# Performance work log

Measured on AMD Instinct MI355X. Metric: run time of the kernel, lower is better.

Reference implementation:

```python
import jax, jax.numpy as jnp
import numpy as np

N_NODES = 100000
N_EDGES = 1600000
IN_FEATS, H_FEATS, NUM_CLASSES = 128, 64, 16


def setup_inputs() -> dict:
    key = jax.random.key(0)
    k1, k2, k3, k4, k5, k6, k7 = jax.random.split(key, 7)
    in_feat = jax.random.normal(k1, (N_NODES, IN_FEATS), dtype=jnp.float32)
    src = jax.random.randint(k2, (N_EDGES,), 0, N_NODES)
    dst = jax.random.randint(k3, (N_EDGES,), 0, N_NODES)
    # GraphConv parameters (glorot-ish scale)
    W1 = jax.random.normal(k4, (IN_FEATS, H_FEATS), dtype=jnp.float32) * (1.0 / np.sqrt(IN_FEATS))
    b1 = jnp.zeros((H_FEATS,), dtype=jnp.float32)
    W2 = jax.random.normal(k5, (H_FEATS, NUM_CLASSES), dtype=jnp.float32) * (1.0 / np.sqrt(H_FEATS))
    b2 = jnp.zeros((NUM_CLASSES,), dtype=jnp.float32)
    return {"in_feat": in_feat, "src": src, "dst": dst, "W1": W1, "b1": b1, "W2": W2, "b2": b2}


def reference(in_feat, src, dst, W1, b1, W2, b2):
    N = in_feat.shape[0]
    ones = jnp.ones(src.shape[0], dtype=in_feat.dtype)
    deg_out = jax.ops.segment_sum(ones, src, num_segments=N)
    deg_in = jax.ops.segment_sum(ones, dst, num_segments=N)
    # norm='both': deg^{-1/2}, degree clamped to >= 1 (allow_zero_in_degree)
    norm_out = jnp.maximum(deg_out, 1.0) ** -0.5  # [N]
    norm_in = jnp.maximum(deg_in, 1.0) ** -0.5    # [N]

    def gconv(x, W, b):
        x = x * norm_out[:, None]          # pre-normalize by src degree
        x = x @ W                          # project first (in_feats >= out_feats)
        msg = x[src]                       # gather [E, d_out]
        agg = jax.ops.segment_sum(msg, dst, num_segments=N)  # scatter-add [N, d_out]
        return agg * norm_in[:, None] + b  # post-normalize + bias

    h = jax.nn.relu(gconv(in_feat, W1, b1))
    h = gconv(h, W2, b2)
    return jnp.mean(h, axis=0)  # dgl.mean_nodes over single graph -> [num_classes]
```

## Files before the change

kernel.cpp:

```cpp
#include <hip/hip_runtime.h>
#include <hip/hip_fp16.h>

#define IN_F 128
#define H_F 64
#define C_F 16
#define BUCKET 256
#define BSH 8
#define MAXB 512
#define EPB 8192
#define AGG_W 64
#define CAP 2048
#define NRED 64
#define AK 136

typedef __attribute__((ext_vector_type(8))) short short8v;
typedef __attribute__((ext_vector_type(4))) float f32x4;

static __device__ inline short f2bf(float f) {
    unsigned u = __float_as_uint(f);
    unsigned r = (u + 0x7FFFu + ((u >> 16) & 1u)) >> 16;
    return (short)r;
}

__global__ __launch_bounds__(256) void k_bhist(const int* __restrict__ src,
                                               const int* __restrict__ dst,
                                               int* __restrict__ cntS,
                                               int* __restrict__ cntD, int E, int nb) {
    __shared__ int hs[MAXB];
    __shared__ int hd[MAXB];
    const int tid = threadIdx.x;
    for (int i = tid; i < MAXB; i += 256) { hs[i] = 0; hd[i] = 0; }
    __syncthreads();
    const int start = blockIdx.x * EPB;
    for (int k = 0; k < EPB / 256; ++k) {
        int e = start + (k << 8) + tid;
        if (e < E) {
            atomicAdd(&hs[src[e] >> BSH], 1);
            atomicAdd(&hd[dst[e] >> BSH], 1);
        }
    }
    __syncthreads();
    for (int b = tid; b < nb; b += 256) {
        int s = hs[b], d = hd[b];
        if (s) atomicAdd(&cntS[b], s);
        if (d) atomicAdd(&cntD[b], d);
    }
}

__global__ __launch_bounds__(1024) void k_bucketscan2(const int* __restrict__ cntD,
                                                      const int* __restrict__ cntS,
                                                      int* __restrict__ baseD,
                                                      int* __restrict__ curD,
                                                      int* __restrict__ baseS,
                                                      int* __restrict__ curS,
                                                      int nb, int E) {
    __shared__ int s[1024];
    const int t = threadIdx.x;
    for (int pass = 0; pass < 2; ++pass) {
        const int* cnt = pass ? cntS : cntD;
        int* base = pass ? baseS : baseD;
        int* cur  = pass ? curS  : curD;
        int i0 = 2 * t, i1 = 2 * t + 1;
        int v0 = (i0 < nb) ? cnt[i0] : 0;
        int v1 = (i1 < nb) ? cnt[i1] : 0;
        int pair = v0 + v1;
        s[t] = pair;
        __syncthreads();
        for (int off = 1; off < 1024; off <<= 1) {
            int x = (t >= off) ? s[t - off] : 0;
            __syncthreads();
            s[t] += x;
            __syncthreads();
        }
        int excl = s[t] - pair;
        if (i0 < nb) { base[i0] = excl;      cur[i0] = excl; }
        if (i1 < nb) { base[i1] = excl + v0; cur[i1] = excl + v0; }
        if (t == 0) base[nb] = E;
        __syncthreads();
    }
}

__global__ __launch_bounds__(256) void k_bin2(const int* __restrict__ src,
                                              const int* __restrict__ dst,
                                              int* __restrict__ gCurD,
                                              int* __restrict__ gCurS,
                                              unsigned int* __restrict__ binnedD,
                                              unsigned int* __restrict__ binnedS,
                                              int E, int nb) {
    __shared__ int hd[MAXB], hs[MAXB];
    __shared__ int bd[MAXB], bs[MAXB];
    __shared__ int cd[MAXB], cs[MAXB];
    const int tid = threadIdx.x;
    const int start = blockIdx.x * EPB;
    for (int i = tid; i < MAXB; i += 256) { hd[i] = 0; hs[i] = 0; cd[i] = 0; cs[i] = 0; }
    __syncthreads();
    for (int k = 0; k < EPB / 256; ++k) {
        int e = start + (k << 8) + tid;
        if (e < E) {
            atomicAdd(&hd[dst[e] >> BSH], 1);
            atomicAdd(&hs[src[e] >> BSH], 1);
        }
    }
    __syncthreads();
    for (int b = tid; b < nb; b += 256) {
        if (hd[b]) bd[b] = atomicAdd(&gCurD[b], hd[b]);
        if (hs[b]) bs[b] = atomicAdd(&gCurS[b], hs[b]);
    }
    __syncthreads();
    for (int k = 0; k < EPB / 256; ++k) {
        int e = start + (k << 8) + tid;
        if (e < E) {
            int sv = src[e], dv = dst[e];
            int b1 = dv >> BSH;
            int p1 = bd[b1] + atomicAdd(&cd[b1], 1);
            binnedD[p1] = ((unsigned)(dv & (BUCKET - 1)) << 17) | (unsigned)sv;
            int b2 = sv >> BSH;
            int p2 = bs[b2] + atomicAdd(&cs[b2], 1);
            binnedS[p2] = ((unsigned)(sv & (BUCKET - 1)) << 17) | (unsigned)dv;
        }
    }
}

__global__ __launch_bounds__(256) void k_sortD(const unsigned int* __restrict__ binnedD,
                                               const int* __restrict__ baseD,
                                               int* __restrict__ sortedSrc,
                                               int* __restrict__ nodeOff,
                                               float* __restrict__ norm_in,
                                               int N, int E) {
    __shared__ int hist[BUCKET];
    __shared__ int cur[BUCKET];
    __shared__ int wtot[4];
    const int tid = threadIdx.x, lane = tid & 63, wave = tid >> 6;
    const int b = blockIdx.x;
    const int s0 = baseD[b], s1 = baseD[b + 1];

    hist[tid] = 0;
    __syncthreads();
    for (int i = s0 + tid; i < s1; i += 256)
        atomicAdd(&hist[binnedD[i] >> 17], 1);
    __syncthreads();

    int v = hist[tid];
    int inc = v;
#pragma unroll
    for (int off = 1; off < 64; off <<= 1) {
        int t2 = __shfl_up(inc, off);
        if (lane >= off) inc += t2;
    }
    if (lane == 63) wtot[wave] = inc;
    __syncthreads();
    int add = 0;
#pragma unroll
    for (int w2 = 0; w2 < 4; ++w2)
        if (w2 < wave) add += wtot[w2];
    int excl = add + inc - v;
    cur[tid] = s0 + excl;
    int gn = b * BUCKET + tid;
    if (gn < N) {
        nodeOff[gn] = s0 + excl;
        norm_in[gn] = 1.0f / sqrtf((float)max(v, 1));
        if (gn == N - 1) nodeOff[N] = E;
    }
    __syncthreads();

    for (int i = s0 + tid; i < s1; i += 256) {
        unsigned c = binnedD[i];
        int p = atomicAdd(&cur[c >> 17], 1);
        sortedSrc[p] = (int)(c & 0x1FFFFu);
    }
}

__global__ __launch_bounds__(256) void k_wsum(const unsigned int* __restrict__ binnedS,
                                              const int* __restrict__ baseS,
                                              const float* __restrict__ norm_in,
                                              float* __restrict__ wsum,
                                              float* __restrict__ norm_out, int N) {
    __shared__ float wloc[BUCKET];
    __shared__ int hist[BUCKET];
    const int tid = threadIdx.x;
    wloc[tid] = 0.0f;
    hist[tid] = 0;
    __syncthreads();
    const int b = blockIdx.x;
    const int s0 = baseS[b], s1 = baseS[b + 1];
    for (int i = s0 + tid; i < s1; i += 256) {
        unsigned c = binnedS[i];
        int sl = (int)(c >> 17);
        float ni = norm_in[c & 0x1FFFFu];
        atomicAdd(&hist[sl], 1);
        atomicAdd(&wloc[sl], ni);
    }
    __syncthreads();
    int gn = b * BUCKET + tid;
    if (gn < N) {
        norm_out[gn] = 1.0f / sqrtf((float)max(hist[tid], 1));
        wsum[gn] = wloc[tid];
    }
}

__global__ __launch_bounds__(256) void k_gemm1(const float* __restrict__ in_feat,
                                               const float* __restrict__ W1,
                                               const float* __restrict__ norm_out,
                                               unsigned char* __restrict__ X1q, int N) {
    __shared__ union {
        short a[64][AK];
        float c[64][68];
    } u;
    __shared__ short wt[64][AK];
    const int t = threadIdx.x;
    const int lane = t & 63, wave = t >> 6;
    const int base = blockIdx.x * 64;

    for (int i = t; i < IN_F * H_F; i += 256) {
        int k = i >> 6, n = i & 63;
        wt[n][k] = f2bf(W1[i]);
    }
    for (int i = t; i < 64 * IN_F / 4; i += 256) {
        int n = i >> 5, k4 = (i & 31) * 4;
        int gn = base + n;
        float4 v = make_float4(0.f, 0.f, 0.f, 0.f);
        if (gn < N) v = *(const float4*)(in_feat + (size_t)gn * IN_F + k4);
        short4 s4 = make_short4(f2bf(v.x), f2bf(v.y), f2bf(v.z), f2bf(v.w));
        *(short4*)&u.a[n][k4] = s4;
    }
    __syncthreads();

    f32x4 acc0 = {}, acc1 = {}, acc2 = {}, acc3 = {};
    const int rowb = wave * 16 + (lane & 15);
    const int ko = (lane >> 4) * 8;
#pragma unroll
    for (int kk = 0; kk < 4; ++kk) {
        short8v af = *(const short8v*)&u.a[rowb][kk * 32 + ko];
        short8v b0 = *(const short8v*)&wt[0 + (lane & 15)][kk * 32 + ko];
        short8v b1f = *(const short8v*)&wt[16 + (lane & 15)][kk * 32 + ko];
        short8v b2 = *(const short8v*)&wt[32 + (lane & 15)][kk * 32 + ko];
        short8v b3 = *(const short8v*)&wt[48 + (lane & 15)][kk * 32 + ko];
        acc0 = __builtin_amdgcn_mfma_f32_16x16x32_bf16(af, b0, acc0, 0, 0, 0);
        acc1 = __builtin_amdgcn_mfma_f32_16x16x32_bf16(af, b1f, acc1, 0, 0, 0);
        acc2 = __builtin_amdgcn_mfma_f32_16x16x32_bf16(af, b2, acc2, 0, 0, 0);
        acc3 = __builtin_amdgcn_mfma_f32_16x16x32_bf16(af, b3, acc3, 0, 0, 0);
    }
    __syncthreads();

    {
        const int col = lane & 15;
        const int row0 = wave * 16 + (lane >> 4) * 4;
#pragma unroll
        for (int r = 0; r < 4; ++r) {
            u.c[row0 + r][col +  0] = acc0[r];
            u.c[row0 + r][col + 16] = acc1[r];
            u.c[row0 + r][col + 32] = acc2[r];
            u.c[row0 + r][col + 48] = acc3[r];
        }
    }
    __syncthreads();

    {
        int n = t >> 2, fq = (t & 3) * 16;
        int gn = base + n;
        if (gn < N) {
            float no = norm_out[gn];
            unsigned pk[4];
#pragma unroll
            for (int q = 0; q < 4; ++q) {
                int f = fq + q * 4;
                int w0 = 0;
                w0 = __builtin_amdgcn_cvt_pk_fp8_f32(u.c[n][f + 0] * no, u.c[n][f + 1] * no, w0, false);
                w0 = __builtin_amdgcn_cvt_pk_fp8_f32(u.c[n][f + 2] * no, u.c[n][f + 3] * no, w0, true);
                pk[q] = (unsigned)w0;
            }
            *(uint4*)&X1q[(size_t)gn * 64 + fq] = make_uint4(pk[0], pk[1], pk[2], pk[3]);
        }
    }
}

__global__ __launch_bounds__(256) void k_agg(const unsigned char* __restrict__ X1q,
                                             const int* __restrict__ sortedSrc,
                                             const int* __restrict__ nodeOff,
                                             const float* __restrict__ norm_in,
                                             const float* __restrict__ norm_out,
                                             const float* __restrict__ wsum,
                                             const float* __restrict__ b1,
                                             float* __restrict__ partials, int N) {
    __shared__ int ids[CAP];
    __shared__ int noff[AGG_W + 1];
    __shared__ float hl[4][64];
    const int tid = threadIdx.x, lane = tid & 63, wave = tid >> 6;
    const int fq = (lane & 15) * 4;
    const int eo = lane >> 4;
    const int gbase = blockIdx.x * AGG_W;
    const int nend = (gbase + AGG_W < N) ? gbase + AGG_W : N;
    const int nloc = nend - gbase;

    if (tid <= nloc) noff[tid] = nodeOff[gbase + tid];
    __syncthreads();
    const int s0 = noff[0];
    const int cnt = noff[nloc] - s0;
    const bool fast = (cnt <= CAP);
    if (fast) {
        for (int i = tid; i < cnt; i += 256) ids[i] = sortedSrc[s0 + i];
    }
    __syncthreads();

    const float bj0 = b1[fq + 0], bj1 = b1[fq + 1];
    const float bj2 = b1[fq + 2], bj3 = b1[fq + 3];
    float h0 = 0.f, h1 = 0.f, h2 = 0.f, h3 = 0.f;

    for (int k = 0; k < 16; ++k) {
        int nl = wave * 16 + k;
        if (nl >= nloc) break;
        int gn = gbase + nl;
        int e0 = noff[nl] - s0, e1 = noff[nl + 1] - s0;
        float a0 = 0.f, a1 = 0.f, a2 = 0.f, a3 = 0.f;
        for (int e = e0; e < e1; e += 16) {
            int sv[4];
            unsigned qv[4];
#pragma unroll
            for (int u = 0; u < 4; ++u) {
                int ee = e + 4 * u + eo;
                sv[u] = (ee < e1) ? (fast ? ids[ee] : sortedSrc[s0 + ee]) : -1;
            }
#pragma unroll
            for (int u = 0; u < 4; ++u)
                qv[u] = (sv[u] >= 0) ? *(const unsigned*)&X1q[(size_t)sv[u] * 64 + fq] : 0u;
#pragma unroll
            for (int u = 0; u < 4; ++u) {
                a0 += __builtin_amdgcn_cvt_f32_fp8(qv[u], 0);
                a1 += __builtin_amdgcn_cvt_f32_fp8(qv[u], 1);
                a2 += __builtin_amdgcn_cvt_f32_fp8(qv[u], 2);
                a3 += __builtin_amdgcn_cvt_f32_fp8(qv[u], 3);
            }
        }
        a0 += __shfl_xor(a0, 16); a0 += __shfl_xor(a0, 32);
        a1 += __shfl_xor(a1, 16); a1 += __shfl_xor(a1, 32);
        a2 += __shfl_xor(a2, 16); a2 += __shfl_xor(a2, 32);
        a3 += __shfl_xor(a3, 16); a3 += __shfl_xor(a3, 32);
        float ni = norm_in[gn];
        float w  = norm_out[gn] * wsum[gn];
        float v0 = a0 * ni + bj0, v1 = a1 * ni + bj1;
        float v2 = a2 * ni + bj2, v3 = a3 * ni + bj3;
        h0 = fmaf(v0 > 0.f ? v0 : 0.f, w, h0);
        h1 = fmaf(v1 > 0.f ? v1 : 0.f, w, h1);
        h2 = fmaf(v2 > 0.f ? v2 : 0.f, w, h2);
        h3 = fmaf(v3 > 0.f ? v3 : 0.f, w, h3);
    }
    if (lane < 16) {
        hl[wave][fq + 0] = h0; hl[wave][fq + 1] = h1;
        hl[wave][fq + 2] = h2; hl[wave][fq + 3] = h3;
    }
    __syncthreads();
    if (wave == 0)
        partials[(size_t)blockIdx.x * 64 + lane] =
            (hl[0][lane] + hl[1][lane]) + (hl[2][lane] + hl[3][lane]);
}

__global__ __launch_bounds__(256) void k_red(const float* __restrict__ partials,
                                             double* __restrict__ red, int nbp) {
    const int lane = threadIdx.x & 63, wave = threadIdx.x >> 6;
    const int rpb = (nbp + NRED - 1) / NRED;
    const int r0 = blockIdx.x * rpb;
    int r1 = r0 + rpb; if (r1 > nbp) r1 = nbp;
    double s = 0.0;
    for (int r = r0 + wave; r < r1; r += 4)
        s += (double)partials[(size_t)r * 64 + lane];
    __shared__ double sd[4][64];
    sd[wave][lane] = s;
    __syncthreads();
    if (wave == 0)
        red[(size_t)blockIdx.x * 64 + lane] =
            (sd[0][lane] + sd[1][lane]) + (sd[2][lane] + sd[3][lane]);
}

__global__ __launch_bounds__(256) void k_final(const double* __restrict__ red,
                                               const float* __restrict__ W2,
                                               const float* __restrict__ b2,
                                               float* __restrict__ out, int N) {
    __shared__ double hs[4][64];
    const int sub = threadIdx.x >> 6;
    const int j   = threadIdx.x & 63;
    double s = 0.0;
    for (int p = sub; p < NRED; p += 4)
        s += red[(size_t)p * 64 + j];
    hs[sub][j] = s;
    __syncthreads();
    if (threadIdx.x < C_F) {
        int c = threadIdx.x;
        double o = 0.0;
        for (int k = 0; k < 64; ++k) {
            double hk = hs[0][k] + hs[1][k] + hs[2][k] + hs[3][k];
            o += hk * (double)W2[k * C_F + c];
        }
        out[c] = (float)(o / (double)N + (double)b2[c]);
    }
}

extern "C" void kernel_launch(void* const* d_in, const int* in_sizes, int n_in,
                              void* d_out, int out_size, void* d_ws, size_t ws_size,
                              hipStream_t stream) {
    const float* in_feat = (const float*)d_in[0];
    const int*   src     = (const int*)d_in[1];
    const int*   dst     = (const int*)d_in[2];
    const float* W1      = (const float*)d_in[3];
    const float* b1      = (const float*)d_in[4];
    const float* W2      = (const float*)d_in[5];
    const float* b2      = (const float*)d_in[6];
    float* out = (float*)d_out;

    const int N = in_sizes[0] / IN_F;
    const int E = in_sizes[1];
    const int nb = (N + BUCKET - 1) / BUCKET;
    const int nBin = (E + EPB - 1) / EPB;
    const int nAgg = (N + AGG_W - 1) / AGG_W;

    char* p = (char*)d_ws;
    auto alloc = [&](size_t bytes, size_t align) -> void* {
        size_t a = ((size_t)p + align - 1) & ~(align - 1);
        p = (char*)(a + bytes);
        return (void*)a;
    };
    unsigned char* X1q = (unsigned char*)alloc(64 * (size_t)N, 16);
    unsigned int* binnedD = (unsigned int*)alloc(4 * (size_t)E, 16);
    unsigned int* binnedS = (unsigned int*)alloc(4 * (size_t)E, 16);
    int*   sortedSrc = (int*)alloc(4 * (size_t)E, 16);
    int*   cntD   = (int*)alloc(4 * MAXB, 16);
    int*   cntS   = (int*)alloc(4 * MAXB, 4);
    int*   baseD  = (int*)alloc(4 * (MAXB + 1), 4);
    int*   curD   = (int*)alloc(4 * MAXB, 4);
    int*   baseS  = (int*)alloc(4 * (MAXB + 1), 4);
    int*   curS   = (int*)alloc(4 * MAXB, 4);
    int*   nodeOff  = (int*)alloc(4 * ((size_t)N + 1), 4);
    float* norm_in  = (float*)alloc(4 * (size_t)N, 4);
    float* norm_out = (float*)alloc(4 * (size_t)N, 4);
    float* wsum     = (float*)alloc(4 * (size_t)N, 4);
    float* partials = (float*)alloc(4 * (size_t)nAgg * 64, 16);
    double* red     = (double*)alloc(8 * (size_t)NRED * 64, 8);

    hipMemsetAsync(cntD, 0, 2 * MAXB * sizeof(int), stream);

    k_bhist<<<nBin, 256, 0, stream>>>(src, dst, cntS, cntD, E, nb);

    k_bucketscan2<<<1, 1024, 0, stream>>>(cntD, cntS, baseD, curD, baseS, curS, nb, E);

    k_bin2<<<nBin, 256, 0, stream>>>(src, dst, curD, curS, binnedD, binnedS, E, nb);

    k_sortD<<<nb, 256, 0, stream>>>(binnedD, baseD, sortedSrc, nodeOff, norm_in, N, E);
    k_wsum <<<nb, 256, 0, stream>>>(binnedS, baseS, norm_in, wsum, norm_out, N);

    k_gemm1<<<(N + 63) / 64, 256, 0, stream>>>(in_feat, W1, norm_out, X1q, N);

    k_agg<<<nAgg, 256, 0, stream>>>(X1q, sortedSrc, nodeOff, norm_in, norm_out,
                                    wsum, b1, partials, N);

    k_red  <<<NRED, 256, 0, stream>>>(partials, red, nAgg);
    k_final<<<1, 256, 0, stream>>>(red, W2, b2, out, N);
}
```

Baseline: 162.0 us.

## Split binning by role, halve histogram chunk, precompute bf16 W1 once

The combined src/dst binning kernel is split into a 2D grid where each block handles one key role, doubling block count and halving shared-memory footprint per block. The histogram kernel processes half as many edges per block for more parallelism. W1 is converted to a transposed bf16 buffer once in a new prep kernel, so each GEMM block no longer converts 8K weights into LDS. Instead the MFMA B operands are read from global memory, which adds one small kernel launch and relies on cache hits for those weight reads.

```diff
diff --git a/kernel.cpp b/kernel.cpp
--- a/kernel.cpp
+++ b/kernel.cpp
@@ -8,6 +8,7 @@
 #define BSH 8
 #define MAXB 512
 #define EPB 8192
+#define EPBH 4096
 #define AGG_W 64
 #define CAP 2048
 #define NRED 64
@@ -20,6 +21,15 @@
     unsigned u = __float_as_uint(f);
     unsigned r = (u + 0x7FFFu + ((u >> 16) & 1u)) >> 16;
     return (short)r;
+}
+
+__global__ __launch_bounds__(256) void k_prep(const float* __restrict__ W1,
+                                              short* __restrict__ wbf) {
+    int i = blockIdx.x * 256 + threadIdx.x;
+    if (i < IN_F * H_F) {
+        int n = i >> 7, k = i & 127;
+        wbf[i] = f2bf(W1[k * H_F + n]);
+    }
 }
 
 __global__ __launch_bounds__(256) void k_bhist(const int* __restrict__ src,
@@ -31,8 +41,8 @@
     const int tid = threadIdx.x;
     for (int i = tid; i < MAXB; i += 256) { hs[i] = 0; hd[i] = 0; }
     __syncthreads();
-    const int start = blockIdx.x * EPB;
-    for (int k = 0; k < EPB / 256; ++k) {
+    const int start = blockIdx.x * EPBH;
+    for (int k = 0; k < EPBH / 256; ++k) {
         int e = start + (k << 8) + tid;
         if (e < E) {
             atomicAdd(&hs[src[e] >> BSH], 1);
@@ -80,43 +90,41 @@
     }
 }
 
-__global__ __launch_bounds__(256) void k_bin2(const int* __restrict__ src,
-                                              const int* __restrict__ dst,
-                                              int* __restrict__ gCurD,
-                                              int* __restrict__ gCurS,
-                                              unsigned int* __restrict__ binnedD,
-                                              unsigned int* __restrict__ binnedS,
-                                              int E, int nb) {
-    __shared__ int hd[MAXB], hs[MAXB];
-    __shared__ int bd[MAXB], bs[MAXB];
-    __shared__ int cd[MAXB], cs[MAXB];
+__global__ __launch_bounds__(256) void k_bin(const int* __restrict__ src,
+                                             const int* __restrict__ dst,
+                                             int* __restrict__ gCurD,
+                                             int* __restrict__ gCurS,
+                                             unsigned int* __restrict__ binnedD,
+                                             unsigned int* __restrict__ binnedS,
+                                             int E, int nb) {
+    __shared__ int hist[MAXB];
+    __shared__ int base[MAXB];
+    __shared__ int cur[MAXB];
     const int tid = threadIdx.x;
+    const bool roleS = blockIdx.y != 0;
+    const int* __restrict__ key = roleS ? src : dst;
+    const int* __restrict__ pay = roleS ? dst : src;
+    int* gCur = roleS ? gCurS : gCurD;
+    unsigned int* out = roleS ? binnedS : binnedD;
     const int start = blockIdx.x * EPB;
-    for (int i = tid; i < MAXB; i += 256) { hd[i] = 0; hs[i] = 0; cd[i] = 0; cs[i] = 0; }
+
+    for (int i = tid; i < MAXB; i += 256) { hist[i] = 0; cur[i] = 0; }
+    __syncthreads();
+    for (int k = 0; k < EPB / 256; ++k) {
+        int e = start + (k << 8) + tid;
+        if (e < E) atomicAdd(&hist[key[e] >> BSH], 1);
+    }
+    __syncthreads();
+    for (int b = tid; b < nb; b += 256)
+        if (hist[b]) base[b] = atomicAdd(&gCur[b], hist[b]);
     __syncthreads();
     for (int k = 0; k < EPB / 256; ++k) {
         int e = start + (k << 8) + tid;
         if (e < E) {
-            atomicAdd(&hd[dst[e] >> BSH], 1);
-            atomicAdd(&hs[src[e] >> BSH], 1);
-        }
-    }
-    __syncthreads();
-    for (int b = tid; b < nb; b += 256) {
-        if (hd[b]) bd[b] = atomicAdd(&gCurD[b], hd[b]);
-        if (hs[b]) bs[b] = atomicAdd(&gCurS[b], hs[b]);
-    }
-    __syncthreads();
-    for (int k = 0; k < EPB / 256; ++k) {
-        int e = start + (k << 8) + tid;
-        if (e < E) {
-            int sv = src[e], dv = dst[e];
-            int b1 = dv >> BSH;
-            int p1 = bd[b1] + atomicAdd(&cd[b1], 1);
-            binnedD[p1] = ((unsigned)(dv & (BUCKET - 1)) << 17) | (unsigned)sv;
-            int b2 = sv >> BSH;
-            int p2 = bs[b2] + atomicAdd(&cs[b2], 1);
-            binnedS[p2] = ((unsigned)(sv & (BUCKET - 1)) << 17) | (unsigned)dv;
+            int kv = key[e];
+            int b = kv >> BSH;
+            int p = base[b] + atomicAdd(&cur[b], 1);
+            out[p] = ((unsigned)(kv & (BUCKET - 1)) << 17) | (unsigned)pay[e];
         }
     }
 }
@@ -199,22 +207,17 @@
 }
 
 __global__ __launch_bounds__(256) void k_gemm1(const float* __restrict__ in_feat,
-                                               const float* __restrict__ W1,
+                                               const short* __restrict__ wbf,
                                                const float* __restrict__ norm_out,
                                                unsigned char* __restrict__ X1q, int N) {
     __shared__ union {
         short a[64][AK];
         float c[64][68];
     } u;
-    __shared__ short wt[64][AK];
     const int t = threadIdx.x;
     const int lane = t & 63, wave = t >> 6;
     const int base = blockIdx.x * 64;
 
-    for (int i = t; i < IN_F * H_F; i += 256) {
-        int k = i >> 6, n = i & 63;
-        wt[n][k] = f2bf(W1[i]);
-    }
     for (int i = t; i < 64 * IN_F / 4; i += 256) {
         int n = i >> 5, k4 = (i & 31) * 4;
         int gn = base + n;
@@ -228,13 +231,14 @@
     f32x4 acc0 = {}, acc1 = {}, acc2 = {}, acc3 = {};
     const int rowb = wave * 16 + (lane & 15);
     const int ko = (lane >> 4) * 8;
+    const int wcol = lane & 15;
 #pragma unroll
     for (int kk = 0; kk < 4; ++kk) {
         short8v af = *(const short8v*)&u.a[rowb][kk * 32 + ko];
-        short8v b0 = *(const short8v*)&wt[0 + (lane & 15)][kk * 32 + ko];
-        short8v b1f = *(const short8v*)&wt[16 + (lane & 15)][kk * 32 + ko];
-        short8v b2 = *(const short8v*)&wt[32 + (lane & 15)][kk * 32 + ko];
-        short8v b3 = *(const short8v*)&wt[48 + (lane & 15)][kk * 32 + ko];
+        short8v b0 = *(const short8v*)&wbf[(size_t)( 0 + wcol) * IN_F + kk * 32 + ko];
+        short8v b1f = *(const short8v*)&wbf[(size_t)(16 + wcol) * IN_F + kk * 32 + ko];
+        short8v b2 = *(const short8v*)&wbf[(size_t)(32 + wcol) * IN_F + kk * 32 + ko];
+        short8v b3 = *(const short8v*)&wbf[(size_t)(48 + wcol) * IN_F + kk * 32 + ko];
         acc0 = __builtin_amdgcn_mfma_f32_16x16x32_bf16(af, b0, acc0, 0, 0, 0);
         acc1 = __builtin_amdgcn_mfma_f32_16x16x32_bf16(af, b1f, acc1, 0, 0, 0);
         acc2 = __builtin_amdgcn_mfma_f32_16x16x32_bf16(af, b2, acc2, 0, 0, 0);
@@ -410,6 +414,7 @@
     const int E = in_sizes[1];
     const int nb = (N + BUCKET - 1) / BUCKET;
     const int nBin = (E + EPB - 1) / EPB;
+    const int nBh  = (E + EPBH - 1) / EPBH;
     const int nAgg = (N + AGG_W - 1) / AGG_W;
 
     char* p = (char*)d_ws;
@@ -419,6 +424,7 @@
         return (void*)a;
     };
     unsigned char* X1q = (unsigned char*)alloc(64 * (size_t)N, 16);
+    short* wbf = (short*)alloc(2 * IN_F * H_F, 16);
     unsigned int* binnedD = (unsigned int*)alloc(4 * (size_t)E, 16);
     unsigned int* binnedS = (unsigned int*)alloc(4 * (size_t)E, 16);
     int*   sortedSrc = (int*)alloc(4 * (size_t)E, 16);
@@ -437,16 +443,18 @@
 
     hipMemsetAsync(cntD, 0, 2 * MAXB * sizeof(int), stream);
 
-    k_bhist<<<nBin, 256, 0, stream>>>(src, dst, cntS, cntD, E, nb);
+    k_prep <<<(IN_F * H_F + 255) / 256, 256, 0, stream>>>(W1, wbf);
+    k_bhist<<<nBh, 256, 0, stream>>>(src, dst, cntS, cntD, E, nb);
 
     k_bucketscan2<<<1, 1024, 0, stream>>>(cntD, cntS, baseD, curD, baseS, curS, nb, E);
 
-    k_bin2<<<nBin, 256, 0, stream>>>(src, dst, curD, curS, binnedD, binnedS, E, nb);
+    dim3 gBin(nBin, 2);
+    k_bin<<<gBin, 256, 0, stream>>>(src, dst, curD, curS, binnedD, binnedS, E, nb);
 
     k_sortD<<<nb, 256, 0, stream>>>(binnedD, baseD, sortedSrc, nodeOff, norm_in, N, E);
     k_wsum <<<nb, 256, 0, stream>>>(binnedS, baseS, norm_in, wsum, norm_out, N);
 
-    k_gemm1<<<(N + 63) / 64, 256, 0, stream>>>(in_feat, W1, norm_out, X1q, N);
+    k_gemm1<<<(N + 63) / 64, 256, 0, stream>>>(in_feat, wbf, norm_out, X1q, N);
 
     k_agg<<<nAgg, 256, 0, stream>>>(X1q, sortedSrc, nodeOff, norm_in, norm_out,
                                     wsum, b1, partials, N);
```

New measurement: 172.9 us. 6.7% more time.
